# Kernel tuning notes

Measured on AMD Instinct MI355X. Metric: run time of the kernel, lower is better.

Reference implementation:

```python
import jax, jax.numpy as jnp
import numpy as np

STRIDES = (2, 2, 2, 2)
ALPHA = 1.0
NEG_SLOPE = 0.1


def _conv1d(h, w, b, stride):
    # h: (N, C, L), w: (O, I, K) -> (N, O, L_out), VALID padding
    out = jax.lax.conv_general_dilated(
        h, w, window_strides=(stride,), padding='VALID',
        dimension_numbers=('NCH', 'OIH', 'NCH'))
    return out + b[None, :, None]


def setup_inputs() -> dict:
    key = jax.random.key(0)
    ks = jax.random.split(key, 10)
    N, C, L = 256, 128, 1024
    k_sizes = (15, 12, 7, 4)
    inp = {'x': jax.random.normal(ks[0], (N, C, L), dtype=jnp.float32)}
    for i, k in enumerate(k_sizes):
        fan_in = C * k
        scale = 1.0 / np.sqrt(fan_in).astype(np.float32)
        inp[f'w{i+1}'] = jax.random.normal(ks[1 + 2 * i], (C, C, k), dtype=jnp.float32) * scale
        inp[f'b{i+1}'] = jax.random.normal(ks[2 + 2 * i], (C,), dtype=jnp.float32) * 0.01
    D = C * 59  # flattened encoder output: 1024->505->247->121->59
    inp['centers'] = jax.random.normal(ks[9], (64, D), dtype=jnp.float32)
    return inp


def reference(x, w1, b1, w2, b2, w3, b3, w4, b4, centers):
    ws = [(w1, b1), (w2, b2), (w3, b3), (w4, b4)]
    h = x
    for i, ((w, b), s) in enumerate(zip(ws, STRIDES)):
        h = _conv1d(h, w, b, s)
        if i != len(ws) - 1:
            h = jnp.where(h > 0, h, NEG_SLOPE * h)  # LeakyReLU(0.1)
    z = h.reshape(h.shape[0], -1)  # (N, D)
    # squared distances via norm expansion: ||z||^2 + ||c||^2 - 2 z.c
    d2 = (jnp.sum(z * z, axis=1, keepdims=True)
          + jnp.sum(centers * centers, axis=1)[None, :]
          - 2.0 * z @ centers.T)  # (N, K)
    q = 1.0 / (1.0 + d2 / ALPHA)
    q = q ** ((ALPHA + 1.0) / 2.0)
    q = q / jnp.sum(q, axis=1, keepdims=True)
    return q
```

## Files before the change

### kernel.cpp

```cpp
#include <hip/hip_runtime.h>

typedef __bf16 bf16;
typedef __bf16 bf16x4 __attribute__((ext_vector_type(4)));
typedef __bf16 bf16x8 __attribute__((ext_vector_type(8)));
typedef float f32x4 __attribute__((ext_vector_type(4)));

#define CCH 128

__global__ void k_prep_wall(const float* __restrict__ w1, const float* __restrict__ w2,
                            const float* __restrict__ w3, const float* __restrict__ w4,
                            bf16* __restrict__ o1, bf16* __restrict__ o2,
                            bf16* __restrict__ o3, bf16* __restrict__ o4) {
    int idx = blockIdx.x * 256 + threadIdx.x;
    const float* src; bf16* dst; int Kw; int r = idx;
    if (r < 15 * 16384) { src = w1; dst = o1; Kw = 15; }
    else if ((r -= 15 * 16384) < 12 * 16384) { src = w2; dst = o2; Kw = 12; }
    else if ((r -= 12 * 16384) < 7 * 16384) { src = w3; dst = o3; Kw = 7; }
    else if ((r -= 7 * 16384) < 4 * 16384) { src = w4; dst = o4; Kw = 4; }
    else return;
    int e = r & 7, lane = (r >> 3) & 63, og = (r >> 9) & 7, c = (r >> 12) & 3, kt = r >> 14;
    int o = og * 16 + (lane & 15);
    int i = c * 32 + (lane >> 4) * 8 + e;
    dst[r] = (bf16)src[(o * 128 + i) * Kw + kt];
}

__global__ __launch_bounds__(256, 8) void k_prep_x(const float* __restrict__ x,
                                                   bf16* __restrict__ xT) {
    constexpr int S = 130;
    __shared__ __align__(16) bf16 lds[64 * S];
    const int n = blockIdx.y;
    const int p0 = blockIdx.x * 64;
    const int tid = threadIdx.x;
#pragma unroll
    for (int it = 0; it < 8; ++it) {
        int u = tid + it * 256;
        int ch = u >> 4;
        int v = u & 15;
        f32x4 t = *(const f32x4*)(x + ((size_t)n * CCH + ch) * 1024 + p0 + v * 4);
#pragma unroll
        for (int e = 0; e < 4; ++e) lds[(v * 4 + e) * S + ch] = (bf16)t[e];
    }
    __syncthreads();
    bf16* op = xT + ((size_t)n * 1024 + p0) * CCH;
#pragma unroll
    for (int it = 0; it < 4; ++it) {
        int u = tid + it * 256;
        int p = u >> 4;
        int g = u & 15;
        *(bf16x8*)(op + p * CCH + g * 8) = *(const bf16x8*)(lds + p * S + g * 8);
    }
}

__global__ void k_prep_c(const float* __restrict__ c, bf16* __restrict__ cbp,
                         float* __restrict__ cc) {
    int k = blockIdx.x;
    int tid = threadIdx.x;
    float s = 0.f;
    for (int idx = tid; idx < 64 * 128; idx += 256) {
        int l = idx >> 7;
        int o = idx & 127;
        float v = (l < 59) ? c[k * 7552 + o * 59 + l] : 0.f;
        bf16 b = (bf16)v;
        cbp[(size_t)k * 64 * 128 + idx] = b;
        float fv = (float)b;
        s += fv * fv;
    }
    __shared__ float red[256];
    red[tid] = s;
    __syncthreads();
    for (int st = 128; st > 0; st >>= 1) {
        if (tid < st) red[tid] += red[tid + st];
        __syncthreads();
    }
    if (tid == 0) cc[k] = red[0];
}

template <int KW, int IN_CAP, int OUT_ROWS, int LT, int PH, bool ACT>
__global__ __launch_bounds__(256, 4) void k_conv(
    const bf16* __restrict__ in_, const bf16* __restrict__ wTp,
    const float* __restrict__ bias, bf16* __restrict__ out) {
    constexpr int P = (LT - 1) * 2 + KW;
    constexpr int CPP = 128 / PH;
    constexpr int KC = CPP / 32;
    constexpr int C16N = CPP / 8;
    constexpr int RS = CPP;
    constexpr int KCL = (KC == 4) ? 2 : 1;
    constexpr int NLT = LT / 16;
    constexpr int ESE = 136;
    constexpr int SMELE = (P * RS > LT * ESE) ? P * RS : LT * ESE;
    constexpr int NJ = KW * KC;
    __shared__ __align__(16) bf16 smem[SMELE];

    const int n = blockIdx.y;
    const int l0 = blockIdx.x * LT;
    const int p0 = l0 * 2;
    const int tid = threadIdx.x;
    const int wid = tid >> 6;
    const int lane = tid & 63;
    const int quad = lane >> 4;
    const int l15 = lane & 15;
    const int og0 = wid * 2;

    f32x4 acc[2][NLT];
#pragma unroll
    for (int a = 0; a < 2; ++a)
#pragma unroll
        for (int b = 0; b < NLT; ++b) acc[a][b] = (f32x4){0.f, 0.f, 0.f, 0.f};

    bf16x8 afr[2][2];
    const bf16* wbase = wTp + (size_t)lane * 8;

    afr[0][0] = *(const bf16x8*)(wbase + ((size_t)(og0 + 0) << 9));
    afr[0][1] = *(const bf16x8*)(wbase + ((size_t)(og0 + 1) << 9));

#pragma unroll 1
    for (int ph = 0; ph < PH; ++ph) {
        if (ph) __syncthreads();

        constexpr int UNITS = P * C16N;
        constexpr int NIT = (UNITS + 255) / 256;
        const bf16* base = in_ + ((size_t)n * IN_CAP + p0) * CCH + ph * CPP;
#pragma unroll
        for (int it = 0; it < NIT; ++it) {
            int u = tid + it * 256;
            if ((UNITS & 255) == 0 || u < UNITS) {
                int p = u >> ((C16N == 16) ? 4 : 3);
                int c = u & (C16N - 1);
                bf16x8 t = *(const bf16x8*)(base + (size_t)p * CCH + c * 8);
                int sc = (PH == 2) ? (c ^ ((p >> 1) & 7))
                                   : ((c & 8) | ((c & 7) ^ ((p >> 1) & 7)));
                *(bf16x8*)(smem + p * RS + sc * 8) = t;
            }
        }
        __syncthreads();

#pragma unroll 2
        for (int j = 0; j < NJ; ++j) {
            int nj = j + 1, nph = ph;
            if (nj == NJ) { nj = 0; ++nph; }
            if (nph < PH) {
                int kt1 = nj >> KCL;
                int c1 = (nj & (KC - 1)) + nph * KC;
                const bf16* wp = wbase + ((size_t)((kt1 * 4 + c1) * 8 + og0) << 9);
                afr[(j + 1) & 1][0] = *(const bf16x8*)(wp);
                afr[(j + 1) & 1][1] = *(const bf16x8*)(wp + 512);
            }
            const int kt = j >> KCL;
            const int c16l = (j & (KC - 1)) * 4 + quad;
#pragma unroll
            for (int lt = 0; lt < NLT; ++lt) {
                int p = (lt * 16 + l15) * 2 + kt;
                int sc = (PH == 2) ? (c16l ^ ((p >> 1) & 7))
                                   : ((c16l & 8) | ((c16l & 7) ^ ((p >> 1) & 7)));
                bf16x8 bfr = *(const bf16x8*)(smem + p * RS + sc * 8);
                acc[0][lt] = __builtin_amdgcn_mfma_f32_16x16x32_bf16(
                    afr[j & 1][0], bfr, acc[0][lt], 0, 0, 0);
                acc[1][lt] = __builtin_amdgcn_mfma_f32_16x16x32_bf16(
                    afr[j & 1][1], bfr, acc[1][lt], 0, 0, 0);
            }
        }
    }

    __syncthreads();
#pragma unroll
    for (int ot = 0; ot < 2; ++ot) {
        const int o0 = wid * 32 + ot * 16 + quad * 4;
        const f32x4 bv = *(const f32x4*)(bias + o0);
#pragma unroll
        for (int lt = 0; lt < NLT; ++lt) {
            const int l = lt * 16 + l15;
            bf16x4 pk;
#pragma unroll
            for (int r = 0; r < 4; ++r) {
                float v = acc[ot][lt][r] + bv[r];
                if (ACT) v = (v > 0.f) ? v : 0.1f * v;
                pk[r] = (bf16)v;
            }
            *(bf16x4*)(smem + l * ESE + o0) = pk;
        }
    }
    __syncthreads();
    constexpr int SNIT = LT * 16 / 256;
    bf16* op = out + ((size_t)n * OUT_ROWS + l0) * CCH;
#pragma unroll
    for (int it = 0; it < SNIT; ++it) {
        int u = tid + it * 256;
        int l = u >> 4;
        int g = u & 15;
        *(bf16x8*)(op + l * CCH + g * 8) = *(const bf16x8*)(smem + l * ESE + g * 8);
    }
}

__global__ __launch_bounds__(256, 2) void k_conv4_dist(
    const bf16* __restrict__ in_, const bf16* __restrict__ wTp,
    const float* __restrict__ bias, const bf16* __restrict__ cbp,
    const float* __restrict__ cc, float* __restrict__ out) {
    constexpr int KW = 4, P = 130, IN_CAP = 128, NJ = 16;
    constexpr int ESE = 136;
    __shared__ __align__(16) bf16 smem[P * 128];
    __shared__ __align__(16) bf16 zmem[64 * ESE];
    __shared__ float red[256];
    __shared__ float qsh[64];

    const int n = blockIdx.x;
    const int tid = threadIdx.x;
    const int wid = tid >> 6;
    const int lane = tid & 63;
    const int quad = lane >> 4;
    const int l15 = lane & 15;
    const int og0 = wid * 2;

    f32x4 acc[2][4];
#pragma unroll
    for (int a = 0; a < 2; ++a)
#pragma unroll
        for (int b = 0; b < 4; ++b) acc[a][b] = (f32x4){0.f, 0.f, 0.f, 0.f};

    bf16x8 afr[2][2];
    const bf16* wbase = wTp + (size_t)lane * 8;
    afr[0][0] = *(const bf16x8*)(wbase + ((size_t)(og0 + 0) << 9));
    afr[0][1] = *(const bf16x8*)(wbase + ((size_t)(og0 + 1) << 9));

    {
        constexpr int UNITS = P * 16;
        const bf16* base = in_ + (size_t)n * IN_CAP * CCH;
#pragma unroll
        for (int it = 0; it < (UNITS + 255) / 256; ++it) {
            int u = tid + it * 256;
            if (u < UNITS) {
                int p = u >> 4;
                int c = u & 15;
                bf16x8 t = *(const bf16x8*)(base + (size_t)p * CCH + c * 8);
                int sc = (c & 8) | ((c & 7) ^ ((p >> 1) & 7));
                *(bf16x8*)(smem + p * 128 + sc * 8) = t;
            }
        }
    }
    __syncthreads();

#pragma unroll 2
    for (int j = 0; j < NJ; ++j) {
        if (j + 1 < NJ) {
            int kt1 = (j + 1) >> 2;
            int c1 = (j + 1) & 3;
            const bf16* wp = wbase + ((size_t)((kt1 * 4 + c1) * 8 + og0) << 9);
            afr[(j + 1) & 1][0] = *(const bf16x8*)(wp);
            afr[(j + 1) & 1][1] = *(const bf16x8*)(wp + 512);
        }
        const int kt = j >> 2;
        const int c16l = (j & 3) * 4 + quad;
#pragma unroll
        for (int lt = 0; lt < 4; ++lt) {
            int p = (lt * 16 + l15) * 2 + kt;
            int sc = (c16l & 8) | ((c16l & 7) ^ ((p >> 1) & 7));
            bf16x8 bfr = *(const bf16x8*)(smem + p * 128 + sc * 8);
            acc[0][lt] = __builtin_amdgcn_mfma_f32_16x16x32_bf16(
                afr[j & 1][0], bfr, acc[0][lt], 0, 0, 0);
            acc[1][lt] = __builtin_amdgcn_mfma_f32_16x16x32_bf16(
                afr[j & 1][1], bfr, acc[1][lt], 0, 0, 0);
        }
    }

    __syncthreads();
#pragma unroll
    for (int ot = 0; ot < 2; ++ot) {
        const int o0 = wid * 32 + ot * 16 + quad * 4;
        const f32x4 bv = *(const f32x4*)(bias + o0);
#pragma unroll
        for (int lt = 0; lt < 4; ++lt) {
            const int l = lt * 16 + l15;
            bf16x4 pk;
#pragma unroll
            for (int r = 0; r < 4; ++r) {
                float v = acc[ot][lt][r] + bv[r];
                pk[r] = (l < 59) ? (bf16)v : (bf16)0.f;
            }
            *(bf16x4*)(zmem + l * ESE + o0) = pk;
        }
    }
    __syncthreads();

    const int kc = tid >> 2;
    const int part = tid & 3;
    const bf16* cr = cbp + ((size_t)kc * 64 + part * 16) * 128;
    const bf16* zr = zmem + part * 16 * ESE;
    float t = 0.f;
#pragma unroll 2
    for (int l = 0; l < 16; ++l) {
#pragma unroll
        for (int g = 0; g < 16; ++g) {
            bf16x8 cv = *(const bf16x8*)(cr + l * 128 + g * 8);
            bf16x8 zv = *(const bf16x8*)(zr + l * ESE + g * 8);
#pragma unroll
            for (int e = 0; e < 8; ++e) {
                float zf = (float)zv[e];
                t += zf * (zf - 2.f * (float)cv[e]);
            }
        }
    }
    red[tid] = t;
    __syncthreads();
    if (tid < 64) {
        float d2 = red[tid * 4] + red[tid * 4 + 1] + red[tid * 4 + 2] + red[tid * 4 + 3]
                   + cc[tid];
        qsh[tid] = 1.f / (1.f + d2);
    }
    __syncthreads();
    if (tid < 64) {
        float q = qsh[tid];
        float tot = q;
        for (int o = 32; o > 0; o >>= 1) tot += __shfl_down(tot, o);
        tot = __shfl(tot, 0);
        out[n * 64 + tid] = q / tot;
    }
}

extern "C" void kernel_launch(void* const* d_in, const int* in_sizes, int n_in,
                              void* d_out, int out_size, void* d_ws, size_t ws_size,
                              hipStream_t stream) {
    (void)in_sizes; (void)n_in; (void)out_size; (void)ws_size;
    const float* x   = (const float*)d_in[0];
    const float* w1  = (const float*)d_in[1];
    const float* b1  = (const float*)d_in[2];
    const float* w2  = (const float*)d_in[3];
    const float* b2  = (const float*)d_in[4];
    const float* w3  = (const float*)d_in[5];
    const float* b3  = (const float*)d_in[6];
    const float* w4  = (const float*)d_in[7];
    const float* b4  = (const float*)d_in[8];
    const float* cen = (const float*)d_in[9];
    float* out = (float*)d_out;

    char* ws = (char*)d_ws;
    size_t off = 0;
    auto alloc = [&](size_t bytes) -> void* {
        void* p = ws + off;
        off += (bytes + 255) & ~(size_t)255;
        return p;
    };
    bf16* wT1 = (bf16*)alloc((size_t)15 * 16384 * sizeof(bf16));
    bf16* wT2 = (bf16*)alloc((size_t)12 * 16384 * sizeof(bf16));
    bf16* wT3 = (bf16*)alloc((size_t)7 * 16384 * sizeof(bf16));
    bf16* wT4 = (bf16*)alloc((size_t)4 * 16384 * sizeof(bf16));
    bf16* cbp = (bf16*)alloc((size_t)64 * 64 * 128 * sizeof(bf16));
    float* cc = (float*)alloc(64 * sizeof(float));
    bf16* h1  = (bf16*)alloc((size_t)256 * 512 * 128 * sizeof(bf16));
    bf16* xT  = (bf16*)alloc((size_t)256 * 1024 * 128 * sizeof(bf16));
    bf16* h2  = xT;
    bf16* h3  = h1;
    (void)alloc((size_t)1 << 20);

    k_prep_wall<<<(38 * 16384 + 255) / 256, 256, 0, stream>>>(w1, w2, w3, w4, wT1, wT2, wT3, wT4);
    k_prep_c<<<64, 256, 0, stream>>>(cen, cbp, cc);
    k_prep_x<<<dim3(16, 256), 256, 0, stream>>>(x, xT);

    k_conv<15, 1024, 512, 128, 2, true>
        <<<dim3(4, 256), 256, 0, stream>>>(xT, wT1, b1, h1);
    k_conv<12, 512, 256, 64, 1, true>
        <<<dim3(4, 256), 256, 0, stream>>>(h1, wT2, b2, h2);
    k_conv<7, 256, 128, 64, 1, true>
        <<<dim3(2, 256), 256, 0, stream>>>(h2, wT3, b3, h3);
    k_conv4_dist<<<256, 256, 0, stream>>>(h3, wT4, b4, cbp, cc, out);
}
```

Before: 383.8 us.

## Widen conv4_dist to 512 threads and restructure distance reduction per wave

Doubles the final conv+distance kernel block to 8 waves, each owning one 16-channel output tile, and drops a barrier before the epilogue. The distance stage now has each wave compute full dot products for one center at a time using coalesced center reads and a wave shuffle reduction, replacing the per-thread partial sums and shared-memory reduction. Conv3 tiles are halved to 32 positions, giving twice as many blocks for more parallelism. In exchange, conv3 reloads more halo input across tiles, and the wider block may limit occupancy.

```diff
diff --git a/kernel.cpp b/kernel.cpp
--- a/kernel.cpp
+++ b/kernel.cpp
@@ -191,16 +191,15 @@
     }
 }
 
-__global__ __launch_bounds__(256, 2) void k_conv4_dist(
+__global__ __launch_bounds__(512, 1) void k_conv4_dist(
     const bf16* __restrict__ in_, const bf16* __restrict__ wTp,
     const float* __restrict__ bias, const bf16* __restrict__ cbp,
     const float* __restrict__ cc, float* __restrict__ out) {
-    constexpr int KW = 4, P = 130, IN_CAP = 128, NJ = 16;
+    constexpr int P = 130, NJ = 16;
     constexpr int ESE = 136;
     __shared__ __align__(16) bf16 smem[P * 128];
     __shared__ __align__(16) bf16 zmem[64 * ESE];
-    __shared__ float red[256];
-    __shared__ float qsh[64];
+    __shared__ float d2s[64];
 
     const int n = blockIdx.x;
     const int tid = threadIdx.x;
@@ -208,25 +207,21 @@
     const int lane = tid & 63;
     const int quad = lane >> 4;
     const int l15 = lane & 15;
-    const int og0 = wid * 2;
-
-    f32x4 acc[2][4];
-#pragma unroll
-    for (int a = 0; a < 2; ++a)
-#pragma unroll
-        for (int b = 0; b < 4; ++b) acc[a][b] = (f32x4){0.f, 0.f, 0.f, 0.f};
-
-    bf16x8 afr[2][2];
+
+    f32x4 acc[4];
+#pragma unroll
+    for (int b = 0; b < 4; ++b) acc[b] = (f32x4){0.f, 0.f, 0.f, 0.f};
+
+    bf16x8 afr[2];
     const bf16* wbase = wTp + (size_t)lane * 8;
-    afr[0][0] = *(const bf16x8*)(wbase + ((size_t)(og0 + 0) << 9));
-    afr[0][1] = *(const bf16x8*)(wbase + ((size_t)(og0 + 1) << 9));
+    afr[0] = *(const bf16x8*)(wbase + ((size_t)wid << 9));
 
     {
         constexpr int UNITS = P * 16;
-        const bf16* base = in_ + (size_t)n * IN_CAP * CCH;
-#pragma unroll
-        for (int it = 0; it < (UNITS + 255) / 256; ++it) {
-            int u = tid + it * 256;
+        const bf16* base = in_ + (size_t)n * 128 * CCH;
+#pragma unroll
+        for (int it = 0; it < 5; ++it) {
+            int u = tid + it * 512;
             if (u < UNITS) {
                 int p = u >> 4;
                 int c = u & 15;
@@ -243,9 +238,8 @@
         if (j + 1 < NJ) {
             int kt1 = (j + 1) >> 2;
             int c1 = (j + 1) & 3;
-            const bf16* wp = wbase + ((size_t)((kt1 * 4 + c1) * 8 + og0) << 9);
-            afr[(j + 1) & 1][0] = *(const bf16x8*)(wp);
-            afr[(j + 1) & 1][1] = *(const bf16x8*)(wp + 512);
+            afr[(j + 1) & 1] =
+                *(const bf16x8*)(wbase + ((size_t)((kt1 * 4 + c1) * 8 + wid) << 9));
         }
         const int kt = j >> 2;
         const int c16l = (j & 3) * 4 + quad;
@@ -254,17 +248,12 @@
             int p = (lt * 16 + l15) * 2 + kt;
             int sc = (c16l & 8) | ((c16l & 7) ^ ((p >> 1) & 7));
             bf16x8 bfr = *(const bf16x8*)(smem + p * 128 + sc * 8);
-            acc[0][lt] = __builtin_amdgcn_mfma_f32_16x16x32_bf16(
-                afr[j & 1][0], bfr, acc[0][lt], 0, 0, 0);
-            acc[1][lt] = __builtin_amdgcn_mfma_f32_16x16x32_bf16(
-                afr[j & 1][1], bfr, acc[1][lt], 0, 0, 0);
-        }
-    }
-
-    __syncthreads();
-#pragma unroll
-    for (int ot = 0; ot < 2; ++ot) {
-        const int o0 = wid * 32 + ot * 16 + quad * 4;
+            acc[lt] = __builtin_amdgcn_mfma_f32_16x16x32_bf16(afr[j & 1], bfr, acc[lt], 0, 0, 0);
+        }
+    }
+
+    {
+        const int o0 = wid * 16 + quad * 4;
         const f32x4 bv = *(const f32x4*)(bias + o0);
 #pragma unroll
         for (int lt = 0; lt < 4; ++lt) {
@@ -272,7 +261,7 @@
             bf16x4 pk;
 #pragma unroll
             for (int r = 0; r < 4; ++r) {
-                float v = acc[ot][lt][r] + bv[r];
+                float v = acc[lt][r] + bv[r];
                 pk[r] = (l < 59) ? (bf16)v : (bf16)0.f;
             }
             *(bf16x4*)(zmem + l * ESE + o0) = pk;
@@ -280,37 +269,34 @@
     }
     __syncthreads();
 
-    const int kc = tid >> 2;
-    const int part = tid & 3;
-    const bf16* cr = cbp + ((size_t)kc * 64 + part * 16) * 128;
-    const bf16* zr = zmem + part * 16 * ESE;
-    float t = 0.f;
-#pragma unroll 2
-    for (int l = 0; l < 16; ++l) {
-#pragma unroll
-        for (int g = 0; g < 16; ++g) {
-            bf16x8 cv = *(const bf16x8*)(cr + l * 128 + g * 8);
-            bf16x8 zv = *(const bf16x8*)(zr + l * ESE + g * 8);
+#pragma unroll 1
+    for (int cp = 0; cp < 8; ++cp) {
+        const int kc = cp * 8 + wid;
+        const bf16* cr = cbp + (size_t)kc * 8192;
+        float t = 0.f;
+#pragma unroll
+        for (int it = 0; it < 16; ++it) {
+            int ci = it * 64 + lane;
+            int l = ci >> 4;
+            int g = ci & 15;
+            bf16x8 cv = *(const bf16x8*)(cr + ci * 8);
+            bf16x8 zv = *(const bf16x8*)(zmem + l * ESE + g * 8);
 #pragma unroll
             for (int e = 0; e < 8; ++e) {
                 float zf = (float)zv[e];
                 t += zf * (zf - 2.f * (float)cv[e]);
             }
         }
-    }
-    red[tid] = t;
+#pragma unroll
+        for (int o = 32; o > 0; o >>= 1) t += __shfl_xor(t, o);
+        if (lane == 0) d2s[kc] = t + cc[kc];
+    }
     __syncthreads();
     if (tid < 64) {
-        float d2 = red[tid * 4] + red[tid * 4 + 1] + red[tid * 4 + 2] + red[tid * 4 + 3]
-                   + cc[tid];
-        qsh[tid] = 1.f / (1.f + d2);
-    }
-    __syncthreads();
-    if (tid < 64) {
-        float q = qsh[tid];
+        float q = 1.f / (1.f + d2s[tid]);
         float tot = q;
-        for (int o = 32; o > 0; o >>= 1) tot += __shfl_down(tot, o);
-        tot = __shfl(tot, 0);
+#pragma unroll
+        for (int o = 32; o > 0; o >>= 1) tot += __shfl_xor(tot, o);
         out[n * 64 + tid] = q / tot;
     }
 }
@@ -358,7 +344,7 @@
         <<<dim3(4, 256), 256, 0, stream>>>(xT, wT1, b1, h1);
     k_conv<12, 512, 256, 64, 1, true>
         <<<dim3(4, 256), 256, 0, stream>>>(h1, wT2, b2, h2);
-    k_conv<7, 256, 128, 64, 1, true>
-        <<<dim3(2, 256), 256, 0, stream>>>(h2, wT3, b3, h3);
-    k_conv4_dist<<<256, 256, 0, stream>>>(h3, wT4, b4, cbp, cc, out);
-}
+    k_conv<7, 256, 128, 32, 1, true>
+        <<<dim3(4, 256), 256, 0, stream>>>(h2, wT3, b3, h3);
+    k_conv4_dist<<<256, 512, 0, stream>>>(h3, wT4, b4, cbp, cc, out);
+}
```

Result: faster. 372.0 us (-3.1%).
